# Optimization experiments

Hardware: AMD Instinct MI355X
Metric: run time of the kernel (lower is better)

Reference implementation:

```python
import jax, jax.numpy as jnp
import numpy as np

CHANNELS = 32


def _mlp(x, W1, b1, W2, b2, W3, b3):
    # FNN: Linear -> ReLU -> Linear -> ReLU -> Linear (last layer linear)
    h = jax.nn.relu(x @ W1 + b1)
    h = jax.nn.relu(h @ W2 + b2)
    return h @ W3 + b3


def setup_inputs() -> dict:
    key = jax.random.key(0)
    ks = jax.random.split(key, 8)
    E = 262144
    C = CHANNELS
    H = 128
    d_in = 4  # 2 * spatial_dim
    d_out = C * (C + 1)  # 1056
    s = lambda fan_in: 1.0 / np.sqrt(fan_in)
    return {
        "pos_i": jax.random.normal(ks[0], (E, 2), jnp.float32),
        "pos_j": jax.random.normal(ks[1], (E, 2), jnp.float32),
        "v_j": jax.random.normal(ks[2], (E, C), jnp.float32),
        "W1": jax.random.normal(ks[3], (d_in, H), jnp.float32) * s(d_in),
        "b1": jnp.zeros((H,), jnp.float32),
        "W2": jax.random.normal(ks[4], (H, H), jnp.float32) * s(H),
        "b2": jnp.zeros((H,), jnp.float32),
        "W3": jax.random.normal(ks[5], (H, d_out), jnp.float32) * s(H),
        "b3": jnp.zeros((d_out,), jnp.float32),
    }


def reference(pos_i, pos_j, v_j, W1, b1, W2, b2, W3, b3):
    C = CHANNELS
    pos_ij = jnp.concatenate((pos_i, pos_j), axis=-1)          # [E, 2*spatial_dim]
    kernel = _mlp(pos_ij, W1, b1, W2, b2, W3, b3)
    kernel = kernel.reshape(-1, C, C + 1)                      # [E, C, C+1]
    mat, bias = kernel[..., :, :-1], kernel[..., :, -1]        # [E,C,C], [E,C]
    return jnp.einsum('eij,ej->ei', mat, v_j) + bias           # [E, C]
```

## Files before the change

### kernel.cpp

```cpp
#include <hip/hip_runtime.h>


#define E_TOTAL 262144
#define EPB 256
#define NBLK (E_TOTAL / EPB)

typedef float f32x4 __attribute__((ext_vector_type(4)));
typedef short s8v  __attribute__((ext_vector_type(8)));

__device__ __forceinline__ unsigned short f2bf(float x) {
  unsigned u = __float_as_uint(x);
  u += 0x7fffu + ((u >> 16) & 1u);
  return (unsigned short)(u >> 16);
}

__global__ void prep_pack(const float* __restrict__ W2, const float* __restrict__ W3,
                          const float* __restrict__ b3,
                          unsigned short* __restrict__ Wg2, unsigned short* __restrict__ W2f,
                          unsigned short* __restrict__ b3f, float* __restrict__ b3c) {
  int idx = blockIdx.x * 256 + threadIdx.x;
  if (idx < 135168) {
    int jj = idx & 7, lane = (idx >> 3) & 63;
    int ksnn = idx >> 9, ks = ksnn & 3, nn = ksnn >> 2;
    int nnt = (nn < 33) ? (2 * nn) : (2 * (nn - 33) + 1);
    int k = ks * 32 + ((lane >> 4) << 3) + jj;
    int col = nnt * 16 + (lane & 15);
    int i = col & 31, j = col >> 5;
    Wg2[idx] = f2bf(W3[k * 1056 + i * 33 + j]);
  }
  if (idx < 16384) {
    int ks = idx >> 12, nt = (idx >> 9) & 7, l = (idx >> 3) & 63, jj = idx & 7;
    int k = ks * 32 + ((l >> 4) << 3) + jj;
    int n = nt * 16 + (l & 15);
    W2f[idx] = f2bf(W2[k * 128 + n]);
  }
  if (idx < 1024) {
    int jj = idx & 7, lane = (idx >> 3) & 63, ih = idx >> 9;
    int j = ((lane >> 4) << 3) + jj, i = ih * 16 + (lane & 15);
    b3f[idx] = f2bf(b3[i * 33 + j]);
  }
  if (idx < 32) b3c[idx] = b3[idx * 33 + 32];
}

template <int IH>
__device__ __forceinline__ void g_chunk(const unsigned short* __restrict__ buf,
                                        const float* __restrict__ vt,
                                        int j0, int lane, int eoff,
                                        const s8v (&af)[4][4], float (&oa)[2][4][4]) {
  const f32x4 zero4 = {0.f, 0.f, 0.f, 0.f};
#pragma unroll
  for (int t = 0; t < 3; ++t) {
    const int j = j0 + t;
    s8v bfr[4];
#pragma unroll
    for (int ks = 0; ks < 4; ++ks)
      bfr[ks] = *(const s8v*)&buf[(t * 4 + ks) * 512 + lane * 8];
    f32x4 p[4];
#pragma unroll
    for (int m = 0; m < 4; ++m) {
      p[m] = __builtin_amdgcn_mfma_f32_16x16x32_bf16(af[m][0], bfr[0], zero4, 0, 0, 0);
#pragma unroll
      for (int ks = 1; ks < 4; ++ks)
        p[m] = __builtin_amdgcn_mfma_f32_16x16x32_bf16(af[m][ks], bfr[ks], p[m], 0, 0, 0);
    }
    const float* vp = vt + j * 260 + eoff;
#pragma unroll
    for (int m = 0; m < 4; ++m) {
      f32x4 vv = *(const f32x4*)(vp + m * 16);
#pragma unroll
      for (int r = 0; r < 4; ++r) oa[IH][m][r] += vv[r] * p[m][r];
    }
  }
}

__global__ __launch_bounds__(256, 2) void fnn_fused(
    const float* __restrict__ pos_i, const float* __restrict__ pos_j,
    const float* __restrict__ vj, const float* __restrict__ W1,
    const float* __restrict__ b1, const float* __restrict__ b2,
    const unsigned short* __restrict__ W2f, const unsigned short* __restrict__ Wg2,
    const unsigned short* __restrict__ b3f, const float* __restrict__ b3c,
    float* __restrict__ out) {
  __shared__ __attribute__((aligned(16))) char smem[60432];
  float* vt = (float*)smem;
  unsigned short* h2n = (unsigned short*)(smem + 34320);
  unsigned short* h1c = (unsigned short*)(smem + 51728);
  unsigned short* Bb  = (unsigned short*)(smem + 34320);

  const int tid = threadIdx.x;
  const int w = tid >> 6, lane = tid & 63, q = lane >> 4, ln = lane & 15;
  const int B0 = blockIdx.x * EPB;
  const int eoff = w * 64 + q * 4;

  {
    const float* vrow = vj + (size_t)(B0 + tid) * 32;
#pragma unroll
    for (int j4 = 0; j4 < 8; ++j4) {
      float4 vv = *(const float4*)(vrow + j4 * 4);
      vt[(j4 * 4 + 0) * 260 + tid] = vv.x;
      vt[(j4 * 4 + 1) * 260 + tid] = vv.y;
      vt[(j4 * 4 + 2) * 260 + tid] = vv.z;
      vt[(j4 * 4 + 3) * 260 + tid] = vv.w;
    }
    vt[32 * 260 + tid] = 1.0f;
  }

  float oa[2][4][4];
  {
    s8v av[4];
#pragma unroll
    for (int m = 0; m < 4; ++m) {
      int e = B0 + w * 64 + m * 16 + ln;
      const float4 va = *(const float4*)(vj + (size_t)e * 32 + q * 8);
      const float4 vb = *(const float4*)(vj + (size_t)e * 32 + q * 8 + 4);
      s8v t;
      t[0] = (short)f2bf(va.x); t[1] = (short)f2bf(va.y);
      t[2] = (short)f2bf(va.z); t[3] = (short)f2bf(va.w);
      t[4] = (short)f2bf(vb.x); t[5] = (short)f2bf(vb.y);
      t[6] = (short)f2bf(vb.z); t[7] = (short)f2bf(vb.w);
      av[m] = t;
    }
#pragma unroll
    for (int ih = 0; ih < 2; ++ih) {
      s8v b3fr = *(const s8v*)(b3f + (ih * 64 + lane) * 8);
      float cbv = b3c[ih * 16 + ln];
      f32x4 ci = {cbv, cbv, cbv, cbv};
#pragma unroll
      for (int m = 0; m < 4; ++m) {
        f32x4 p = __builtin_amdgcn_mfma_f32_16x16x32_bf16(av[m], b3fr, ci, 0, 0, 0);
#pragma unroll
        for (int r = 0; r < 4; ++r) oa[ih][m][r] = p[r];
      }
    }
  }

  const int hh0 = (tid & 15) * 8;
  float w1r[4][8], b1r[8];
#pragma unroll
  for (int d = 0; d < 4; ++d)
#pragma unroll
    for (int u = 0; u < 8; ++u) w1r[d][u] = W1[d * 128 + hh0 + u];
#pragma unroll
  for (int u = 0; u < 8; ++u) b1r[u] = b1[hh0 + u];

  s8v af[4][4];
  for (int qtr = 0; qtr < 4; ++qtr) {
    for (int cb = 0; cb < 2; ++cb) {
#pragma unroll
      for (int half = 0; half < 2; ++half) {
        int ee = (tid >> 4) + half * 16;
        int eg = B0 + qtr * 64 + cb * 32 + ee;
        float2 pi = *(const float2*)(pos_i + (size_t)eg * 2);
        float2 pj = *(const float2*)(pos_j + (size_t)eg * 2);
        s8v hv;
#pragma unroll
        for (int u = 0; u < 8; ++u) {
          float o = b1r[u] + pi.x * w1r[0][u] + pi.y * w1r[1][u] +
                    pj.x * w1r[2][u] + pj.y * w1r[3][u];
          hv[u] = (short)f2bf(fmaxf(o, 0.f));
        }
        *(s8v*)&h1c[ee * 136 + hh0] = hv;
      }
      __syncthreads();
#pragma unroll
      for (int s = 0; s < 4; ++s) {
        int tt = w * 4 + s, mt = tt >> 3, nt = tt & 7;
        f32x4 a4 = {0.f, 0.f, 0.f, 0.f};
#pragma unroll
        for (int ks = 0; ks < 4; ++ks) {
          s8v afr = *(const s8v*)&h1c[(mt * 16 + ln) * 136 + ks * 32 + q * 8];
          s8v bfr = *(const s8v*)(W2f + ((ks * 8 + nt) * 64 + lane) * 8);
          a4 = __builtin_amdgcn_mfma_f32_16x16x32_bf16(afr, bfr, a4, 0, 0, 0);
        }
        float b2v = b2[nt * 16 + ln];
        int eb = cb * 32 + mt * 16 + q * 4;
        int kc = nt * 16 + ln;
#pragma unroll
        for (int r = 0; r < 4; ++r)
          h2n[(eb + r) * 136 + kc] = f2bf(fmaxf(a4[r] + b2v, 0.f));
      }
      __syncthreads();
    }
    if (w == qtr) {
#pragma unroll
      for (int m = 0; m < 4; ++m)
#pragma unroll
        for (int ks = 0; ks < 4; ++ks)
          af[m][ks] = *(const s8v*)&h2n[(m * 16 + ln) * 136 + ks * 32 + q * 8];
    }
    __syncthreads();
  }

  s8v pre[3];
#pragma unroll
  for (int t = 0; t < 3; ++t) pre[t] = *(const s8v*)(Wg2 + (t * 256 + tid) * 8);
#pragma unroll
  for (int t = 0; t < 3; ++t) *(s8v*)&Bb[(t * 256 + tid) * 8] = pre[t];
  __syncthreads();

  for (int c = 0; c < 22; ++c) {
    const int bb = c & 1;
    const unsigned short* buf = Bb + bb * 6144;
    if (c + 1 < 22) {
#pragma unroll
      for (int t = 0; t < 3; ++t)
        pre[t] = *(const s8v*)(Wg2 + (c + 1) * 6144 + (t * 256 + tid) * 8);
    }
    if (c < 11) g_chunk<0>(buf, vt, c * 3, lane, eoff, af, oa);
    else        g_chunk<1>(buf, vt, (c - 11) * 3, lane, eoff, af, oa);
    if (c + 1 < 22) {
      unsigned short* nb = Bb + (bb ^ 1) * 6144;
#pragma unroll
      for (int t = 0; t < 3; ++t) *(s8v*)&nb[(t * 256 + tid) * 8] = pre[t];
    }
    __syncthreads();
  }

#pragma unroll
  for (int m = 0; m < 4; ++m)
#pragma unroll
    for (int ih = 0; ih < 2; ++ih)
#pragma unroll
      for (int r = 0; r < 4; ++r) {
        int e = B0 + w * 64 + m * 16 + q * 4 + r;
        out[(size_t)e * 32 + ih * 16 + ln] = oa[ih][m][r];
      }
}

extern "C" void kernel_launch(void* const* d_in, const int* in_sizes, int n_in,
                              void* d_out, int out_size, void* d_ws, size_t ws_size,
                              hipStream_t stream) {
  const float* pos_i = (const float*)d_in[0];
  const float* pos_j = (const float*)d_in[1];
  const float* vj    = (const float*)d_in[2];
  const float* W1    = (const float*)d_in[3];
  const float* b1    = (const float*)d_in[4];
  const float* W2    = (const float*)d_in[5];
  const float* b2    = (const float*)d_in[6];
  const float* W3    = (const float*)d_in[7];
  const float* b3    = (const float*)d_in[8];
  float* outp = (float*)d_out;

  unsigned short* Wg2 = (unsigned short*)d_ws;
  unsigned short* W2f = (unsigned short*)((char*)d_ws + 270336);
  unsigned short* b3f = (unsigned short*)((char*)d_ws + 303104);
  float*          b3c = (float*)((char*)d_ws + 305152);

  prep_pack<<<528, 256, 0, stream>>>(W2, W3, b3, Wg2, W2f, b3f, b3c);
  fnn_fused<<<NBLK, 256, 0, stream>>>(pos_i, pos_j, vj, W1, b1, b2, W2f, Wg2, b3f, b3c, outp);
}
```

Measured before the change: 189.2 us.

## Stream W3 fragments straight from global into registers and raise occupancy

The layer-3 weight tiles are no longer staged through a double-buffered LDS region guarded by a block barrier on every chunk. Each wave now loads its B fragments directly from global memory into three rotating register buffers, software-pipelined two tiles ahead. This drops the per-chunk barrier and LDS round-trip and shrinks shared memory, so launch bounds are raised from two to four blocks per CU. The v_j transpose is moved after the MLP so its buffer can reuse the same LDS. The costs are more redundant L2/L1 traffic, since every block re-reads all of W3, and much tighter register limits that could force spills. The final prefetches read two tiles past the end of Wg2, but those values are never used.

```diff
diff --git a/kernel.cpp b/kernel.cpp
--- a/kernel.cpp
+++ b/kernel.cpp
@@ -42,67 +42,47 @@
   if (idx < 32) b3c[idx] = b3[idx * 33 + 32];
 }
 
+__device__ __forceinline__ void tile_load(s8v (&dst)[4], const unsigned short* __restrict__ Wg2,
+                                          int n, int lane) {
+  const s8v* src = (const s8v*)(Wg2 + (size_t)n * 2048 + lane * 8);
+#pragma unroll
+  for (int ks = 0; ks < 4; ++ks) dst[ks] = src[ks * 64];
+}
+
 template <int IH>
-__device__ __forceinline__ void g_chunk(const unsigned short* __restrict__ buf,
-                                        const float* __restrict__ vt,
-                                        int j0, int lane, int eoff,
-                                        const s8v (&af)[4][4], float (&oa)[2][4][4]) {
+__device__ __forceinline__ void tile_compute(const s8v (&bf)[4], const float* __restrict__ vt,
+                                             int j, int eoff,
+                                             const s8v (&af)[4][4], float (&oa)[2][4][4]) {
   const f32x4 zero4 = {0.f, 0.f, 0.f, 0.f};
-#pragma unroll
-  for (int t = 0; t < 3; ++t) {
-    const int j = j0 + t;
-    s8v bfr[4];
-#pragma unroll
-    for (int ks = 0; ks < 4; ++ks)
-      bfr[ks] = *(const s8v*)&buf[(t * 4 + ks) * 512 + lane * 8];
-    f32x4 p[4];
-#pragma unroll
-    for (int m = 0; m < 4; ++m) {
-      p[m] = __builtin_amdgcn_mfma_f32_16x16x32_bf16(af[m][0], bfr[0], zero4, 0, 0, 0);
-#pragma unroll
-      for (int ks = 1; ks < 4; ++ks)
-        p[m] = __builtin_amdgcn_mfma_f32_16x16x32_bf16(af[m][ks], bfr[ks], p[m], 0, 0, 0);
-    }
-    const float* vp = vt + j * 260 + eoff;
-#pragma unroll
-    for (int m = 0; m < 4; ++m) {
-      f32x4 vv = *(const f32x4*)(vp + m * 16);
-#pragma unroll
-      for (int r = 0; r < 4; ++r) oa[IH][m][r] += vv[r] * p[m][r];
-    }
-  }
-}
-
-__global__ __launch_bounds__(256, 2) void fnn_fused(
+  const float* vp = vt + j * 260 + eoff;
+#pragma unroll
+  for (int m = 0; m < 4; ++m) {
+    f32x4 p = __builtin_amdgcn_mfma_f32_16x16x32_bf16(af[m][0], bf[0], zero4, 0, 0, 0);
+#pragma unroll
+    for (int ks = 1; ks < 4; ++ks)
+      p = __builtin_amdgcn_mfma_f32_16x16x32_bf16(af[m][ks], bf[ks], p, 0, 0, 0);
+    f32x4 vv = *(const f32x4*)(vp + m * 16);
+#pragma unroll
+    for (int r = 0; r < 4; ++r) oa[IH][m][r] += vv[r] * p[r];
+  }
+}
+
+__global__ __launch_bounds__(256, 4) void fnn_fused(
     const float* __restrict__ pos_i, const float* __restrict__ pos_j,
     const float* __restrict__ vj, const float* __restrict__ W1,
     const float* __restrict__ b1, const float* __restrict__ b2,
     const unsigned short* __restrict__ W2f, const unsigned short* __restrict__ Wg2,
     const unsigned short* __restrict__ b3f, const float* __restrict__ b3c,
     float* __restrict__ out) {
-  __shared__ __attribute__((aligned(16))) char smem[60432];
+  __shared__ __attribute__((aligned(16))) char smem[34320];
   float* vt = (float*)smem;
-  unsigned short* h2n = (unsigned short*)(smem + 34320);
-  unsigned short* h1c = (unsigned short*)(smem + 51728);
-  unsigned short* Bb  = (unsigned short*)(smem + 34320);
+  unsigned short* h2n = (unsigned short*)smem;
+  unsigned short* h1c = (unsigned short*)(smem + 17408);
 
   const int tid = threadIdx.x;
   const int w = tid >> 6, lane = tid & 63, q = lane >> 4, ln = lane & 15;
   const int B0 = blockIdx.x * EPB;
   const int eoff = w * 64 + q * 4;
-
-  {
-    const float* vrow = vj + (size_t)(B0 + tid) * 32;
-#pragma unroll
-    for (int j4 = 0; j4 < 8; ++j4) {
-      float4 vv = *(const float4*)(vrow + j4 * 4);
-      vt[(j4 * 4 + 0) * 260 + tid] = vv.x;
-      vt[(j4 * 4 + 1) * 260 + tid] = vv.y;
-      vt[(j4 * 4 + 2) * 260 + tid] = vv.z;
-      vt[(j4 * 4 + 3) * 260 + tid] = vv.w;
-    }
-    vt[32 * 260 + tid] = 1.0f;
-  }
 
   float oa[2][4][4];
   {
@@ -190,29 +170,43 @@
     __syncthreads();
   }
 
-  s8v pre[3];
-#pragma unroll
-  for (int t = 0; t < 3; ++t) pre[t] = *(const s8v*)(Wg2 + (t * 256 + tid) * 8);
-#pragma unroll
-  for (int t = 0; t < 3; ++t) *(s8v*)&Bb[(t * 256 + tid) * 8] = pre[t];
+  {
+    const float* vrow = vj + (size_t)(B0 + tid) * 32;
+#pragma unroll
+    for (int j4 = 0; j4 < 8; ++j4) {
+      float4 vv = *(const float4*)(vrow + j4 * 4);
+      vt[(j4 * 4 + 0) * 260 + tid] = vv.x;
+      vt[(j4 * 4 + 1) * 260 + tid] = vv.y;
+      vt[(j4 * 4 + 2) * 260 + tid] = vv.z;
+      vt[(j4 * 4 + 3) * 260 + tid] = vv.w;
+    }
+    vt[32 * 260 + tid] = 1.0f;
+  }
+
+  s8v bA[4], bB[4], bC[4];
+  tile_load(bA, Wg2, 0, lane);
+  tile_load(bB, Wg2, 1, lane);
   __syncthreads();
 
-  for (int c = 0; c < 22; ++c) {
-    const int bb = c & 1;
-    const unsigned short* buf = Bb + bb * 6144;
-    if (c + 1 < 22) {
-#pragma unroll
-      for (int t = 0; t < 3; ++t)
-        pre[t] = *(const s8v*)(Wg2 + (c + 1) * 6144 + (t * 256 + tid) * 8);
-    }
-    if (c < 11) g_chunk<0>(buf, vt, c * 3, lane, eoff, af, oa);
-    else        g_chunk<1>(buf, vt, (c - 11) * 3, lane, eoff, af, oa);
-    if (c + 1 < 22) {
-      unsigned short* nb = Bb + (bb ^ 1) * 6144;
-#pragma unroll
-      for (int t = 0; t < 3; ++t) *(s8v*)&nb[(t * 256 + tid) * 8] = pre[t];
-    }
-    __syncthreads();
+#pragma unroll 1
+  for (int c = 0; c < 11; ++c) {
+    const int n = c * 3;
+    tile_load(bC, Wg2, n + 2, lane);
+    tile_compute<0>(bA, vt, n + 0, eoff, af, oa);
+    tile_load(bA, Wg2, n + 3, lane);
+    tile_compute<0>(bB, vt, n + 1, eoff, af, oa);
+    tile_load(bB, Wg2, n + 4, lane);
+    tile_compute<0>(bC, vt, n + 2, eoff, af, oa);
+  }
+#pragma unroll 1
+  for (int c = 0; c < 11; ++c) {
+    const int n = 33 + c * 3;
+    tile_load(bC, Wg2, n + 2, lane);
+    tile_compute<1>(bA, vt, n - 33 + 0, eoff, af, oa);
+    tile_load(bA, Wg2, n + 3, lane);
+    tile_compute<1>(bB, vt, n - 33 + 1, eoff, af, oa);
+    tile_load(bB, Wg2, n + 4, lane);
+    tile_compute<1>(bC, vt, n - 33 + 2, eoff, af, oa);
   }
 
 #pragma unroll
```

After: 487.3 us. 2.58x slower.
